# Performance work log

Hardware: AMD Instinct MI355X
Metric: run time of the kernel (lower is better)

Reference implementation:

```python
import jax, jax.numpy as jnp
import numpy as np

DEG = 7
RANK = 8
B = 2_000_000

def setup_inputs() -> dict:
    key = jax.random.key(0)
    k_x, k0, k1, k2, k3 = jax.random.split(key, 5)
    d1 = DEG + 1
    # xavier_normal std = sqrt(2 / (fan_in + fan_out)); for 3D cores torch uses
    # fan_in = rank*(deg+1) style flattening, but any gaussian init is fine for a
    # numerical reference; use std matching 2D xavier on the (first, last) dims.
    def xavier(k, shape):
        fan_in, fan_out = shape[0], shape[-1]
        std = np.sqrt(2.0 / (fan_in + fan_out))
        return jax.random.normal(k, shape, dtype=jnp.float32) * std
    return {
        "X": jax.random.normal(k_x, (B, 4), dtype=jnp.float32),
        "G0": xavier(k0, (d1, RANK)),
        "G1": xavier(k1, (RANK, d1, RANK)),
        "G2": xavier(k2, (RANK, d1, RANK)),
        "G3": xavier(k3, (RANK, d1)),
    }

def reference(X, G0, G1, G2, G3):
    # poly bases: P[b, dim, p] = X[b, dim] ** p, p = 0..deg
    exps = jnp.arange(DEG + 1)               # [d1]
    P = X[:, :, None] ** exps                # [B, 4, d1]
    # chained TT contraction, left to right (avoids any large intermediate)
    t = jnp.einsum('bd,dr->br', P[:, 0], G0)           # [B, r]
    t = jnp.einsum('br,rds,bd->bs', t, G1, P[:, 1])    # [B, r]
    t = jnp.einsum('bs,sdt,bd->bt', t, G2, P[:, 2])    # [B, r]
    res = jnp.einsum('bt,td,bd->b', t, G3, P[:, 3])    # [B]
    return res.reshape(-1, 1)
```

## Files before the change

### kernel.cpp

```cpp
#include <hip/hip_runtime.h>
#include <hip/hip_bf16.h>

#define D1 8
#define RANK 8

typedef float f32x4 __attribute__((ext_vector_type(4)));
typedef short bf16x8 __attribute__((ext_vector_type(8)));

__device__ inline unsigned cvt_pk_bf16(float lo, float hi) {
    unsigned r;
    asm("v_cvt_pk_bf16_f32 %0, %1, %2" : "=v"(r) : "v"(lo), "v"(hi));
    return r;
}

union FragU { unsigned u[4]; bf16x8 v; };

__device__ inline bf16x8 pack8(const float f[8]) {
    FragU x;
    x.u[0] = cvt_pk_bf16(f[0], f[1]);
    x.u[1] = cvt_pk_bf16(f[2], f[3]);
    x.u[2] = cvt_pk_bf16(f[4], f[5]);
    x.u[3] = cvt_pk_bf16(f[6], f[7]);
    return x.v;
}

__device__ inline bf16x8 splat8(float v) {
    FragU x;
    unsigned p = cvt_pk_bf16(v, v);
    x.u[0] = p; x.u[1] = p; x.u[2] = p; x.u[3] = p;
    return x.v;
}

__device__ inline void build_b(const float* __restrict__ G, int col, int grp,
                               bf16x8* Bh, bf16x8* Bl) {
    #pragma unroll
    for (int q = 0; q < 2; ++q) {
        FragU hi, lo;
        #pragma unroll
        for (int pr = 0; pr < 4; ++pr) {
            float v0 = 0.f, v1 = 0.f;
            if (col < 8) {
                v0 = G[(32*q + 8*grp + 2*pr    ) * 8 + col];
                v1 = G[(32*q + 8*grp + 2*pr + 1) * 8 + col];
            }
            float h0 = __bfloat162float(__float2bfloat16(v0));
            float h1 = __bfloat162float(__float2bfloat16(v1));
            hi.u[pr] = cvt_pk_bf16(h0, h1);
            lo.u[pr] = cvt_pk_bf16(v0 - h0, v1 - h1);
        }
        Bh[q] = hi.v;
        Bl[q] = lo.v;
    }
}

#define POWERS(p, xx)                                              \
    p[0] = 1.f;  p[1] = (xx);      p[2] = p[1]*p[1];               \
    p[3] = p[2]*p[1]; p[4] = p[2]*p[2]; p[5] = p[4]*p[1];          \
    p[6] = p[4]*p[2]; p[7] = p[4]*p[3];

__global__ __launch_bounds__(256) void tt_poly_kernel(
    const float* __restrict__ X,
    const float* __restrict__ G0,
    const float* __restrict__ G1,
    const float* __restrict__ G2,
    const float* __restrict__ G3,
    float* __restrict__ out,
    int B, int NW)
{
    __shared__ float L[4][RANK][68];

    const int tid  = threadIdx.x;
    const int w    = tid >> 6;
    const int lane = tid & 63;
    const int col  = lane & 15;
    const int grp  = lane >> 4;

    int rowLbl[4], colLbl[4];
    {
        bf16x8 ones = splat8(1.f);
        bf16x8 lbl  = splat8((float)col);
        f32x4 pr = {0.f, 0.f, 0.f, 0.f};
        f32x4 pc = {0.f, 0.f, 0.f, 0.f};
        pr = __builtin_amdgcn_mfma_f32_16x16x32_bf16(lbl, ones, pr, 0, 0, 0);
        pc = __builtin_amdgcn_mfma_f32_16x16x32_bf16(ones, lbl, pc, 0, 0, 0);
        #pragma unroll
        for (int j = 0; j < 4; ++j) {
            rowLbl[j] = (int)(pr[j] * 0.03125f + 0.5f);
            colLbl[j] = (int)(pc[j] * 0.03125f + 0.5f);
        }
    }

    bf16x8 B1h[2], B1l[2], B2h[2], B2l[2];
    build_b(G1, col, grp, B1h, B1l);
    build_b(G2, col, grp, B2h, B2l);

    float* Lw = &L[w][0][0];
    const int gw = blockIdx.x * 4 + w;

    #pragma unroll 1
    for (int it = 0; it < 4; ++it) {
        const int b = (it * NW + gw) * 64 + lane;
        float4 xv = make_float4(0.f, 0.f, 0.f, 0.f);
        if (b < B) xv = reinterpret_cast<const float4*>(X)[b];

        {
            float p[8];
            POWERS(p, xv.x)
            #pragma unroll
            for (int r = 0; r < 8; ++r) {
                float t = 0.f;
                #pragma unroll
                for (int d = 0; d < 8; ++d)
                    t = fmaf(p[d], G0[d*8 + r], t);
                Lw[r*68 + lane] = t;
            }
        }

        #pragma unroll 1
        for (int g4 = 0; g4 < 4; ++g4) {
            {
                float x1 = __shfl(xv.y, g4*16 + col, 64);
                float p[8];
                POWERS(p, x1)
                float ta = Lw[grp*68     + g4*16 + col];
                float tb = Lw[(grp+4)*68 + g4*16 + col];
                float f0[8], f1[8];
                #pragma unroll
                for (int e = 0; e < 8; ++e) { f0[e] = ta*p[e]; f1[e] = tb*p[e]; }
                bf16x8 a0 = pack8(f0), a1 = pack8(f1);
                f32x4 acc = {0.f, 0.f, 0.f, 0.f};
                acc = __builtin_amdgcn_mfma_f32_16x16x32_bf16(a0, B1h[0], acc, 0, 0, 0);
                acc = __builtin_amdgcn_mfma_f32_16x16x32_bf16(a0, B1l[0], acc, 0, 0, 0);
                acc = __builtin_amdgcn_mfma_f32_16x16x32_bf16(a1, B1h[1], acc, 0, 0, 0);
                acc = __builtin_amdgcn_mfma_f32_16x16x32_bf16(a1, B1l[1], acc, 0, 0, 0);
                #pragma unroll
                for (int j = 0; j < 4; ++j)
                    if (colLbl[j] < 8)
                        Lw[colLbl[j]*68 + g4*16 + rowLbl[j]] = acc[j];
            }
            {
                float x2 = __shfl(xv.z, g4*16 + col, 64);
                float p[8];
                POWERS(p, x2)
                float ta = Lw[grp*68     + g4*16 + col];
                float tb = Lw[(grp+4)*68 + g4*16 + col];
                float f0[8], f1[8];
                #pragma unroll
                for (int e = 0; e < 8; ++e) { f0[e] = ta*p[e]; f1[e] = tb*p[e]; }
                bf16x8 a0 = pack8(f0), a1 = pack8(f1);
                f32x4 acc = {0.f, 0.f, 0.f, 0.f};
                acc = __builtin_amdgcn_mfma_f32_16x16x32_bf16(a0, B2h[0], acc, 0, 0, 0);
                acc = __builtin_amdgcn_mfma_f32_16x16x32_bf16(a0, B2l[0], acc, 0, 0, 0);
                acc = __builtin_amdgcn_mfma_f32_16x16x32_bf16(a1, B2h[1], acc, 0, 0, 0);
                acc = __builtin_amdgcn_mfma_f32_16x16x32_bf16(a1, B2l[1], acc, 0, 0, 0);
                #pragma unroll
                for (int j = 0; j < 4; ++j)
                    if (colLbl[j] < 8)
                        Lw[colLbl[j]*68 + g4*16 + rowLbl[j]] = acc[j];
            }
        }

        {
            float p[8];
            POWERS(p, xv.w)
            float res = 0.f;
            #pragma unroll
            for (int t = 0; t < 8; ++t) {
                float wt = 0.f;
                #pragma unroll
                for (int d = 0; d < 8; ++d)
                    wt = fmaf(p[d], G3[t*8 + d], wt);
                res = fmaf(Lw[t*68 + lane], wt, res);
            }
            if (b < B) out[b] = res;
        }
    }
}

extern "C" void kernel_launch(void* const* d_in, const int* in_sizes, int n_in,
                              void* d_out, int out_size, void* d_ws, size_t ws_size,
                              hipStream_t stream) {
    const float* X  = (const float*)d_in[0];
    const float* G0 = (const float*)d_in[1];
    const float* G1 = (const float*)d_in[2];
    const float* G2 = (const float*)d_in[3];
    const float* G3 = (const float*)d_in[4];
    float* out = (float*)d_out;

    int B = in_sizes[0] / 4;
    int block = 256;
    int grid = (B + block * 4 - 1) / (block * 4);
    int NW = grid * 4;
    tt_poly_kernel<<<grid, block, 0, stream>>>(X, G0, G1, G2, G3, out, B, NW);
}
```

Before: 39.36 us.

## Transpose per-wave LDS state to row-major with vector stores and separate stage buffers

Replaces the rank-major LDS scratch with a sample-major layout (stride 12), so each lane writes its G0 result as two float4 stores and stashes x1/x2 alongside, removing the shuffles. The G1 and G2 stages now write into separate buffers with block-wide __syncthreads between stages, and the g4 loops are fully unrolled. The final stage reads the rank vector with two vector loads. The added block barriers can stall waves that previously ran independently, and the stride-12 layout may introduce LDS bank conflicts.

```diff
diff --git a/kernel.cpp b/kernel.cpp
--- a/kernel.cpp
+++ b/kernel.cpp
@@ -1,18 +1,14 @@
 #include <hip/hip_runtime.h>
 #include <hip/hip_bf16.h>
 
-#define D1 8
-#define RANK 8
-
 typedef float f32x4 __attribute__((ext_vector_type(4)));
 typedef short bf16x8 __attribute__((ext_vector_type(8)));
 
-__device__ inline unsigned cvt_pk_bf16(float lo, float hi) {
+__device__ inline unsigned cvt_pk_bf16(float a, float b) {
     unsigned r;
-    asm("v_cvt_pk_bf16_f32 %0, %1, %2" : "=v"(r) : "v"(lo), "v"(hi));
+    asm("v_cvt_pk_bf16_f32 %0, %1, %2" : "=v"(r) : "v"(a), "v"(b));
     return r;
 }
-
 union FragU { unsigned u[4]; bf16x8 v; };
 
 __device__ inline bf16x8 pack8(const float f[8]) {
@@ -58,6 +54,8 @@
     p[3] = p[2]*p[1]; p[4] = p[2]*p[2]; p[5] = p[4]*p[1];          \
     p[6] = p[4]*p[2]; p[7] = p[4]*p[3];
 
+#define ROWW 12
+
 __global__ __launch_bounds__(256) void tt_poly_kernel(
     const float* __restrict__ X,
     const float* __restrict__ G0,
@@ -67,7 +65,7 @@
     float* __restrict__ out,
     int B, int NW)
 {
-    __shared__ float L[4][RANK][68];
+    __shared__ float L[4][3][64 * ROWW];
 
     const int tid  = threadIdx.x;
     const int w    = tid >> 6;
@@ -94,7 +92,9 @@
     build_b(G1, col, grp, B1h, B1l);
     build_b(G2, col, grp, B2h, B2l);
 
-    float* Lw = &L[w][0][0];
+    float* T0 = &L[w][0][0];
+    float* T1 = &L[w][1][0];
+    float* T2 = &L[w][2][0];
     const int gw = blockIdx.x * 4 + w;
 
     #pragma unroll 1
@@ -106,71 +106,85 @@
         {
             float p[8];
             POWERS(p, xv.x)
-            #pragma unroll
-            for (int r = 0; r < 8; ++r) {
-                float t = 0.f;
+            f32x4 tlo, thi;
+            #pragma unroll
+            for (int r = 0; r < 4; ++r) {
+                float ta = 0.f, tb = 0.f;
                 #pragma unroll
-                for (int d = 0; d < 8; ++d)
-                    t = fmaf(p[d], G0[d*8 + r], t);
-                Lw[r*68 + lane] = t;
+                for (int d = 0; d < 8; ++d) {
+                    ta = fmaf(p[d], G0[d*8 + r    ], ta);
+                    tb = fmaf(p[d], G0[d*8 + r + 4], tb);
+                }
+                tlo[r] = ta; thi[r] = tb;
             }
-        }
-
-        #pragma unroll 1
+            *reinterpret_cast<f32x4*>(&T0[lane*ROWW    ]) = tlo;
+            *reinterpret_cast<f32x4*>(&T0[lane*ROWW + 4]) = thi;
+            *reinterpret_cast<float2*>(&T0[lane*ROWW + 8]) = make_float2(xv.y, xv.z);
+        }
+        __syncthreads();
+
+        #pragma unroll
         for (int g4 = 0; g4 < 4; ++g4) {
-            {
-                float x1 = __shfl(xv.y, g4*16 + col, 64);
-                float p[8];
-                POWERS(p, x1)
-                float ta = Lw[grp*68     + g4*16 + col];
-                float tb = Lw[(grp+4)*68 + g4*16 + col];
-                float f0[8], f1[8];
-                #pragma unroll
-                for (int e = 0; e < 8; ++e) { f0[e] = ta*p[e]; f1[e] = tb*p[e]; }
-                bf16x8 a0 = pack8(f0), a1 = pack8(f1);
-                f32x4 acc = {0.f, 0.f, 0.f, 0.f};
-                acc = __builtin_amdgcn_mfma_f32_16x16x32_bf16(a0, B1h[0], acc, 0, 0, 0);
-                acc = __builtin_amdgcn_mfma_f32_16x16x32_bf16(a0, B1l[0], acc, 0, 0, 0);
-                acc = __builtin_amdgcn_mfma_f32_16x16x32_bf16(a1, B1h[1], acc, 0, 0, 0);
-                acc = __builtin_amdgcn_mfma_f32_16x16x32_bf16(a1, B1l[1], acc, 0, 0, 0);
-                #pragma unroll
-                for (int j = 0; j < 4; ++j)
-                    if (colLbl[j] < 8)
-                        Lw[colLbl[j]*68 + g4*16 + rowLbl[j]] = acc[j];
-            }
-            {
-                float x2 = __shfl(xv.z, g4*16 + col, 64);
-                float p[8];
-                POWERS(p, x2)
-                float ta = Lw[grp*68     + g4*16 + col];
-                float tb = Lw[(grp+4)*68 + g4*16 + col];
-                float f0[8], f1[8];
-                #pragma unroll
-                for (int e = 0; e < 8; ++e) { f0[e] = ta*p[e]; f1[e] = tb*p[e]; }
-                bf16x8 a0 = pack8(f0), a1 = pack8(f1);
-                f32x4 acc = {0.f, 0.f, 0.f, 0.f};
-                acc = __builtin_amdgcn_mfma_f32_16x16x32_bf16(a0, B2h[0], acc, 0, 0, 0);
-                acc = __builtin_amdgcn_mfma_f32_16x16x32_bf16(a0, B2l[0], acc, 0, 0, 0);
-                acc = __builtin_amdgcn_mfma_f32_16x16x32_bf16(a1, B2h[1], acc, 0, 0, 0);
-                acc = __builtin_amdgcn_mfma_f32_16x16x32_bf16(a1, B2l[1], acc, 0, 0, 0);
-                #pragma unroll
-                for (int j = 0; j < 4; ++j)
-                    if (colLbl[j] < 8)
-                        Lw[colLbl[j]*68 + g4*16 + rowLbl[j]] = acc[j];
-            }
-        }
+            const int base = (g4*16 + col) * ROWW;
+            float ta = T0[base + grp];
+            float tb = T0[base + grp + 4];
+            float x1 = T0[base + 8];
+            float p[8];
+            POWERS(p, x1)
+            float f0[8], f1[8];
+            #pragma unroll
+            for (int e = 0; e < 8; ++e) { f0[e] = ta*p[e]; f1[e] = tb*p[e]; }
+            bf16x8 a0 = pack8(f0), a1 = pack8(f1);
+            f32x4 acc = {0.f, 0.f, 0.f, 0.f};
+            acc = __builtin_amdgcn_mfma_f32_16x16x32_bf16(a0, B1h[0], acc, 0, 0, 0);
+            acc = __builtin_amdgcn_mfma_f32_16x16x32_bf16(a0, B1l[0], acc, 0, 0, 0);
+            acc = __builtin_amdgcn_mfma_f32_16x16x32_bf16(a1, B1h[1], acc, 0, 0, 0);
+            acc = __builtin_amdgcn_mfma_f32_16x16x32_bf16(a1, B1l[1], acc, 0, 0, 0);
+            #pragma unroll
+            for (int j = 0; j < 4; ++j)
+                if (colLbl[j] < 8)
+                    T1[(g4*16 + rowLbl[j])*ROWW + colLbl[j]] = acc[j];
+        }
+        __syncthreads();
+
+        #pragma unroll
+        for (int g4 = 0; g4 < 4; ++g4) {
+            const int base = (g4*16 + col) * ROWW;
+            float tc = T1[base + grp];
+            float td = T1[base + grp + 4];
+            float x2 = T0[base + 9];
+            float p[8];
+            POWERS(p, x2)
+            float f0[8], f1[8];
+            #pragma unroll
+            for (int e = 0; e < 8; ++e) { f0[e] = tc*p[e]; f1[e] = td*p[e]; }
+            bf16x8 a0 = pack8(f0), a1 = pack8(f1);
+            f32x4 acc = {0.f, 0.f, 0.f, 0.f};
+            acc = __builtin_amdgcn_mfma_f32_16x16x32_bf16(a0, B2h[0], acc, 0, 0, 0);
+            acc = __builtin_amdgcn_mfma_f32_16x16x32_bf16(a0, B2l[0], acc, 0, 0, 0);
+            acc = __builtin_amdgcn_mfma_f32_16x16x32_bf16(a1, B2h[1], acc, 0, 0, 0);
+            acc = __builtin_amdgcn_mfma_f32_16x16x32_bf16(a1, B2l[1], acc, 0, 0, 0);
+            #pragma unroll
+            for (int j = 0; j < 4; ++j)
+                if (colLbl[j] < 8)
+                    T2[(g4*16 + rowLbl[j])*ROWW + colLbl[j]] = acc[j];
+        }
+        __syncthreads();
 
         {
+            f32x4 u0 = *reinterpret_cast<const f32x4*>(&T2[lane*ROWW    ]);
+            f32x4 u1 = *reinterpret_cast<const f32x4*>(&T2[lane*ROWW + 4]);
             float p[8];
             POWERS(p, xv.w)
             float res = 0.f;
             #pragma unroll
-            for (int t = 0; t < 8; ++t) {
-                float wt = 0.f;
+            for (int t8 = 0; t8 < 8; ++t8) {
+                float wt = G3[t8*8];
                 #pragma unroll
-                for (int d = 0; d < 8; ++d)
-                    wt = fmaf(p[d], G3[t*8 + d], wt);
-                res = fmaf(Lw[t*68 + lane], wt, res);
+                for (int d = 1; d < 8; ++d)
+                    wt = fmaf(p[d], G3[t8*8 + d], wt);
+                float tv = (t8 < 4) ? u0[t8] : u1[t8 - 4];
+                res = fmaf(tv, wt, res);
             }
             if (b < B) out[b] = res;
         }
@@ -189,7 +203,7 @@
 
     int B = in_sizes[0] / 4;
     int block = 256;
-    int grid = (B + block * 4 - 1) / (block * 4);
+    int grid = (B + 1023) / 1024;
     int NW = grid * 4;
     tt_poly_kernel<<<grid, block, 0, stream>>>(X, G0, G1, G2, G3, out, B, NW);
 }
```

Result: slower. 42.01 us (+6.7%).
